# Performance work log

Hardware: AMD Instinct MI355X
Metric: run time of the kernel (lower is better)

## Reference

```python
import jax, jax.numpy as jnp
import numpy as np

D_MODEL = 1024
N_HEADS = 16
HEAD_DIM = D_MODEL // N_HEADS


def setup_inputs() -> dict:
    key = jax.random.key(0)
    ks = jax.random.split(key, 11)
    B, S = 4, 2048
    scale = 1.0 / np.sqrt(D_MODEL)
    inp = {
        "query": jax.random.normal(ks[0], (B, S, D_MODEL), jnp.float32),
        "key": jax.random.normal(ks[1], (B, S, D_MODEL), jnp.float32),
        "value": jax.random.normal(ks[2], (B, S, D_MODEL), jnp.float32),
        "Wq": jax.random.normal(ks[3], (D_MODEL, D_MODEL), jnp.float32) * scale,
        "bq": jnp.zeros((D_MODEL,), jnp.float32),
        "Wk": jax.random.normal(ks[4], (D_MODEL, D_MODEL), jnp.float32) * scale,
        "bk": jnp.zeros((D_MODEL,), jnp.float32),
        "Wv": jax.random.normal(ks[5], (D_MODEL, D_MODEL), jnp.float32) * scale,
        "bv": jnp.zeros((D_MODEL,), jnp.float32),
        "Wo": jax.random.normal(ks[6], (D_MODEL, D_MODEL), jnp.float32) * scale,
        "bo": jnp.zeros((D_MODEL,), jnp.float32),
    }
    return inp


def reference(query, key, value, Wq, bq, Wk, bk, Wv, bv, Wo, bo):
    B, S, _ = query.shape
    # QKV projections (nn.Linear: x @ W.T + b; weights here stored as [out,in])
    q = query @ Wq.T + bq
    k = key @ Wk.T + bk
    v = value @ Wv.T + bv
    # [B, S, H, Dh] -> [B, H, S, Dh]
    q = q.reshape(B, S, N_HEADS, HEAD_DIM).transpose(0, 2, 1, 3)
    k = k.reshape(B, S, N_HEADS, HEAD_DIM).transpose(0, 2, 1, 3)
    v = v.reshape(B, S, N_HEADS, HEAD_DIM).transpose(0, 2, 1, 3)
    # full score matrix [B, H, S, S]
    scores = jnp.einsum("bhqd,bhkd->bhqk", q, k) / jnp.sqrt(
        jnp.asarray(HEAD_DIM, q.dtype)
    )
    attn = jax.nn.softmax(scores, axis=-1)
    out = jnp.einsum("bhqk,bhkd->bhqd", attn, v)  # [B, H, S, Dh]
    out = out.transpose(0, 2, 1, 3).reshape(B, S, D_MODEL)
    return out @ Wo.T + bo
```

## Files before the change

### kernel.cpp

```cpp
#include <hip/hip_runtime.h>
#include <cstdint>
#include <cstddef>


typedef _Float16 h16;
typedef _Float16 h16x4 __attribute__((ext_vector_type(4)));
typedef _Float16 h16x8 __attribute__((ext_vector_type(8)));
typedef __fp16 fp16x2v __attribute__((ext_vector_type(2)));
typedef float f32x4 __attribute__((ext_vector_type(4)));
typedef float f32x16 __attribute__((ext_vector_type(16)));

#define SEQ 2048
#define HDIM 64

__device__ __forceinline__ void gld16(const void* g, void* l) {
  __builtin_amdgcn_global_load_lds((__attribute__((address_space(1))) void*)g,
                                   (__attribute__((address_space(3))) void*)l,
                                   16, 0, 0);
}

#define VMCNT_(n) asm volatile("s_waitcnt vmcnt(" #n ")" ::: "memory")
#define VMCNT(n) VMCNT_(n)

__device__ __forceinline__ void pl32swap(unsigned& a, unsigned& b) {
  asm volatile("v_permlane32_swap_b32 %0, %1" : "+v"(a), "+v"(b));
}

struct CvtArgs {
  const float* src[7];
  h16* dst[7];
  int n4[7];
};

__global__ __launch_bounds__(256) void cvt_kernel(CvtArgs a) {
  const int tk = blockIdx.y;
  const int n4 = a.n4[tk];
  const float4* s = (const float4*)a.src[tk];
  h16x4* d = (h16x4*)a.dst[tk];
  const int stride = gridDim.x * blockDim.x;
  for (int i = blockIdx.x * blockDim.x + threadIdx.x; i < n4; i += stride) {
    float4 v = s[i];
    h16x4 o = {(h16)v.x, (h16)v.y, (h16)v.z, (h16)v.w};
    d[i] = o;
  }
}

enum { EPI_Q = 0, EPI_V = 1, EPI_OUT = 2, EPI_K = 3 };

struct GemmArgs {
  const h16* A[3];
  const h16* W[3];
  const float* bias[3];
  void* dst[3];
  float scale[3];
  int epi[3];
};

__global__ __launch_bounds__(256) void gemm_h16(GemmArgs g) {
  const int z = blockIdx.z;
  const h16* A = g.A[z];
  const h16* W = g.W[z];
  const float* bias = g.bias[z];
  void* dst = g.dst[z];
  const float scale = g.scale[z];
  const int epi = g.epi[z];

  __shared__ __align__(16) h16 sA[128 * 32];
  __shared__ __align__(16) h16 sW[128 * 32];

  const int t = threadIdx.x;
  const int lane = t & 63, wave = t >> 6;
  const int lq = lane & 15, quad = lane >> 4;
  const int wm = wave & 1, wn = wave >> 1;
  const int m0 = blockIdx.y * 128, n0 = blockIdx.x * 128;

  const int srow = wave * 32 + (lane >> 2);
  const int scol = (lane & 3) * 8;
  const h16* Ag = A + (size_t)(m0 + srow) * 1024 + scol;
  const h16* Wg = W + (size_t)(n0 + srow) * 1024 + scol;
  h16* lA = &sA[(wave * 32) * 32];
  h16* lW = &sW[(wave * 32) * 32];

  f32x4 zero4 = {0.f, 0.f, 0.f, 0.f};
  f32x4 acc[4][4];
#pragma unroll
  for (int i = 0; i < 4; ++i)
#pragma unroll
    for (int j = 0; j < 4; ++j) acc[i][j] = zero4;

  for (int k0 = 0; k0 < 1024; k0 += 32) {
    __syncthreads();
    gld16(Ag + k0, lA);
    gld16(Ag + k0 + 16 * 1024, lA + 16 * 32);
    gld16(Wg + k0, lW);
    gld16(Wg + k0 + 16 * 1024, lW + 16 * 32);
    __syncthreads();

    h16x8 af[4], wf[4];
#pragma unroll
    for (int mt = 0; mt < 4; ++mt)
      af[mt] = *(const h16x8*)&sA[(wm * 64 + mt * 16 + lq) * 32 + quad * 8];
#pragma unroll
    for (int nt = 0; nt < 4; ++nt)
      wf[nt] = *(const h16x8*)&sW[(wn * 64 + nt * 16 + lq) * 32 + quad * 8];
#pragma unroll
    for (int mt = 0; mt < 4; ++mt)
#pragma unroll
      for (int nt = 0; nt < 4; ++nt)
        acc[mt][nt] = __builtin_amdgcn_mfma_f32_16x16x32_f16(
            af[mt], wf[nt], acc[mt][nt], 0, 0, 0);
  }

  const int gmb = m0 + wm * 64;
  const int gnb = n0 + wn * 64;
#pragma unroll
  for (int mt = 0; mt < 4; ++mt) {
#pragma unroll
    for (int nt = 0; nt < 4; ++nt) {
      const int gn = gnb + nt * 16 + lq;
      const float bv = bias[gn];
#pragma unroll
      for (int r = 0; r < 4; ++r) {
        const int gm = gmb + mt * 16 + quad * 4 + r;
        const float v = (acc[mt][nt][r] + bv) * scale;
        if (epi == EPI_OUT) {
          ((float*)dst)[(size_t)gm * 1024 + gn] = v;
        } else if (epi == EPI_Q) {
          const int b = gm >> 11, s = gm & 2047, h = gn >> 6, d = gn & 63;
          ((h16*)dst)[((size_t)(b * 16 + h) * 2048 + s) * 64 + d] = (h16)v;
        } else if (epi == EPI_K) {
          const int b = gm >> 11, s = gm & 2047, h = gn >> 6, d = gn & 63;
          const int dsw = (((d >> 3) ^ (s & 7)) << 3) | (d & 7);
          ((h16*)dst)[((size_t)(b * 16 + h) * 2048 + s) * 64 + dsw] = (h16)v;
        } else {
          const int b = gm >> 11, s = gm & 2047, h = gn >> 6, d = gn & 63;
          const int ssw =
              (s & ~127) | (((((s >> 3) & 15) ^ (d & 15))) << 3) | (s & 7);
          ((h16*)dst)[((size_t)(b * 16 + h) * 64 + d) * 2048 + ssw] = (h16)v;
        }
      }
    }
  }
}

__global__ __launch_bounds__(512, 2) void flash_fwd(
    const h16* __restrict__ Qp, const h16* __restrict__ Kp,
    const h16* __restrict__ Vtp, h16* __restrict__ attn) {
  __shared__ __align__(16) h16 sK[2][8192];
  __shared__ __align__(16) h16 sVt[2][8192];

  const int t = threadIdx.x, lane = t & 63, wave = t >> 6;
  const int l31 = lane & 31;
  const int h = lane >> 5;

  const int lin = blockIdx.x + (blockIdx.y << 3);
  const int nid = (lin & 7) * 64 + (lin >> 3);
  const int bh = nid >> 3, q0 = (nid & 7) * 256;

  const h16* Qh = Qp + (size_t)bh * SEQ * HDIM;
  const h16* Kh = Kp + (size_t)bh * SEQ * HDIM;
  const h16* Vh = Vtp + (size_t)bh * HDIM * SEQ;

  const int qrow = q0 + wave * 32 + l31;
  h16x8 bq[4];
#pragma unroll
  for (int ks = 0; ks < 4; ++ks)
    bq[ks] = *(const h16x8*)(Qh + (size_t)qrow * 64 + ks * 16 + h * 8);
  VMCNT(0);
  __builtin_amdgcn_sched_barrier(0);

  const int vr = lane >> 4;
  const int vc = (lane & 15) * 8;

  int colK[4], colV[8];
#pragma unroll
  for (int ks = 0; ks < 4; ++ks) colK[ks] = ((ks * 2 + h) ^ (l31 & 7)) * 8;
#pragma unroll
  for (int ks = 0; ks < 8; ++ks) colV[ks] = ((ks * 2 + h) ^ (l31 & 15)) * 8;

#define STAGE(SLOT, KT)                                                       \
  {                                                                           \
    const h16* gK = Kh + (size_t)(KT) * 64;                                   \
    gld16(gK + wave * 512 + lane * 8, &sK[SLOT][wave * 512]);                 \
    gld16(gK + (wave + 8) * 512 + lane * 8, &sK[SLOT][(wave + 8) * 512]);     \
    gld16(Vh + (size_t)(4 * wave + vr) * SEQ + (KT) + vc,                     \
          &sVt[SLOT][wave * 512]);                                            \
    gld16(Vh + (size_t)(4 * (wave + 8) + vr) * SEQ + (KT) + vc,               \
          &sVt[SLOT][(wave + 8) * 512]);                                      \
  }

  f32x16 zero16 = {};
  f32x16 oT[2];
  oT[0] = zero16;
  oT[1] = zero16;
  float lsum = 0.f;

#define COMPUTE(SLOT)                                                         \
  {                                                                           \
    _Pragma("unroll") for (int mt = 0; mt < 4; ++mt) {                        \
      f32x16 s = zero16;                                                      \
      __builtin_amdgcn_s_setprio(1);                                          \
      _Pragma("unroll") for (int ks = 0; ks < 4; ++ks) {                      \
        h16x8 ak =                                                            \
            *(const h16x8*)&sK[SLOT][(mt * 32 + l31) * 64 + colK[ks]];        \
        s = __builtin_amdgcn_mfma_f32_32x32x16_f16(ak, bq[ks], s, 0, 0, 0);   \
      }                                                                       \
      __builtin_amdgcn_s_setprio(0);                                          \
      uint2 pk[4];                                                            \
      _Pragma("unroll") for (int g = 0; g < 4; ++g) {                         \
        const float e0 = __builtin_amdgcn_exp2f(s[g * 4 + 0]);                \
        const float e1 = __builtin_amdgcn_exp2f(s[g * 4 + 1]);                \
        const float e2 = __builtin_amdgcn_exp2f(s[g * 4 + 2]);                \
        const float e3 = __builtin_amdgcn_exp2f(s[g * 4 + 3]);                \
        lsum += (e0 + e1) + (e2 + e3);                                        \
        fp16x2v c0 = __builtin_amdgcn_cvt_pkrtz(e0, e1);                      \
        fp16x2v c1 = __builtin_amdgcn_cvt_pkrtz(e2, e3);                      \
        pk[g].x = __builtin_bit_cast(unsigned, c0);                           \
        pk[g].y = __builtin_bit_cast(unsigned, c1);                           \
      }                                                                       \
      _Pragma("unroll") for (int ks2 = 0; ks2 < 2; ++ks2) {                   \
        const int ks = mt * 2 + ks2;                                          \
        unsigned ax = pk[2 * ks2].x, ay = pk[2 * ks2].y;                      \
        unsigned bx = pk[2 * ks2 + 1].x, by = pk[2 * ks2 + 1].y;              \
        pl32swap(ax, bx);                                                     \
        pl32swap(ay, by);                                                     \
        uint4 bp32 = {ax, ay, bx, by};                                        \
        h16x8 bp = __builtin_bit_cast(h16x8, bp32);                           \
        __builtin_amdgcn_s_setprio(1);                                        \
        _Pragma("unroll") for (int dt = 0; dt < 2; ++dt) {                    \
          h16x8 av =                                                          \
              *(const h16x8*)&sVt[SLOT][(dt * 32 + l31) * 128 + colV[ks]];    \
          oT[dt] = __builtin_amdgcn_mfma_f32_32x32x16_f16(av, bp, oT[dt], 0,  \
                                                          0, 0);              \
        }                                                                     \
        __builtin_amdgcn_s_setprio(0);                                       \
      }                                                                       \
    }                                                                         \
  }

  STAGE(0, 0);
  STAGE(1, 128);

#pragma unroll 1
  for (int ti = 0; ti < 15; ++ti) {
    VMCNT(4);
    __builtin_amdgcn_s_barrier();
    __builtin_amdgcn_sched_barrier(0);
    const int slot = ti & 1;
    COMPUTE(slot);
    __builtin_amdgcn_sched_barrier(0);
    __builtin_amdgcn_s_barrier();
    if (ti < 14) STAGE(slot, (ti + 2) * 128);
  }
  VMCNT(0);
  __builtin_amdgcn_s_barrier();
  __builtin_amdgcn_sched_barrier(0);
  COMPUTE(1);

#undef STAGE
#undef COMPUTE

  lsum += __shfl_xor(lsum, 32);
  const float inv = 1.f / lsum;

  const int b = bh >> 4, head = bh & 15;
  h16* orow = attn + ((size_t)(b * SEQ + qrow)) * 1024 + head * 64;
#pragma unroll
  for (int dt = 0; dt < 2; ++dt) {
#pragma unroll
    for (int g = 0; g < 4; ++g) {
      h16x4 ov = {(h16)(oT[dt][g * 4 + 0] * inv), (h16)(oT[dt][g * 4 + 1] * inv),
                  (h16)(oT[dt][g * 4 + 2] * inv), (h16)(oT[dt][g * 4 + 3] * inv)};
      *(h16x4*)&orow[dt * 32 + g * 8 + h * 4] = ov;
    }
  }
}

extern "C" void kernel_launch(void* const* d_in, const int* in_sizes, int n_in,
                              void* d_out, int out_size, void* d_ws,
                              size_t ws_size, hipStream_t stream) {
  (void)in_sizes; (void)n_in; (void)out_size;

  const float* query = (const float*)d_in[0];
  const float* key   = (const float*)d_in[1];
  const float* value = (const float*)d_in[2];
  const float* Wq = (const float*)d_in[3];
  const float* bq = (const float*)d_in[4];
  const float* Wk = (const float*)d_in[5];
  const float* bk = (const float*)d_in[6];
  const float* Wv = (const float*)d_in[7];
  const float* bv = (const float*)d_in[8];
  const float* Wo = (const float*)d_in[9];
  const float* bo = (const float*)d_in[10];

  char* ws = (char*)d_ws;
  const size_t MB = 1024 * 1024;
  h16* xq = (h16*)(ws);
  h16* xk = (h16*)(ws + 16 * MB);
  h16* xv = (h16*)(ws + 32 * MB);
  h16* qperm = (h16*)(ws + 48 * MB);
  h16 *kperm, *vperm, *attn, *w16;
  const bool fused = ws_size >= 104 * MB;
  if (fused) {
    kperm = (h16*)(ws + 64 * MB);
    vperm = (h16*)(ws + 80 * MB);
    w16   = (h16*)(ws + 96 * MB);
    attn  = (h16*)(ws);
  } else {
    kperm = (h16*)(ws);
    vperm = (h16*)(ws + 16 * MB);
    attn  = (h16*)(ws + 32 * MB);
    w16   = (h16*)(ws + 64 * MB);
  }
  h16* wq16 = w16;
  h16* wk16 = w16 + 1048576;
  h16* wv16 = w16 + 2 * 1048576;
  h16* wo16 = w16 + 3 * 1048576;

  CvtArgs ca;
  const float* csrc[7] = {query, key, value, Wq, Wk, Wv, Wo};
  h16* cdst[7] = {xq, xk, xv, wq16, wk16, wv16, wo16};
  const int cn4[7] = {2097152, 2097152, 2097152, 262144, 262144, 262144, 262144};
  for (int i = 0; i < 7; ++i) { ca.src[i] = csrc[i]; ca.dst[i] = cdst[i]; ca.n4[i] = cn4[i]; }
  cvt_kernel<<<dim3(512, 7), 256, 0, stream>>>(ca);

  const float qscale = 0.125f * 1.4426950408889634f;
  if (fused) {
    GemmArgs ga;
    ga.A[0] = xq; ga.A[1] = xk; ga.A[2] = xv;
    ga.W[0] = wq16; ga.W[1] = wk16; ga.W[2] = wv16;
    ga.bias[0] = bq; ga.bias[1] = bk; ga.bias[2] = bv;
    ga.dst[0] = qperm; ga.dst[1] = kperm; ga.dst[2] = vperm;
    ga.scale[0] = qscale; ga.scale[1] = 1.f; ga.scale[2] = 1.f;
    ga.epi[0] = EPI_Q; ga.epi[1] = EPI_K; ga.epi[2] = EPI_V;
    gemm_h16<<<dim3(8, 64, 3), 256, 0, stream>>>(ga);
  } else {
    const h16* As[3] = {xq, xk, xv};
    const h16* Ws[3] = {wq16, wk16, wv16};
    const float* bs[3] = {bq, bk, bv};
    h16* ds[3] = {qperm, kperm, vperm};
    const float scl[3] = {qscale, 1.f, 1.f};
    const int ep[3] = {EPI_Q, EPI_K, EPI_V};
    for (int i = 0; i < 3; ++i) {
      GemmArgs ga;
      for (int j = 0; j < 3; ++j) {
        ga.A[j] = As[i]; ga.W[j] = Ws[i]; ga.bias[j] = bs[i];
        ga.dst[j] = ds[i]; ga.scale[j] = scl[i]; ga.epi[j] = ep[i];
      }
      gemm_h16<<<dim3(8, 64, 1), 256, 0, stream>>>(ga);
    }
  }

  flash_fwd<<<dim3(8, 64), 512, 0, stream>>>(qperm, kperm, vperm, attn);

  GemmArgs go;
  for (int j = 0; j < 3; ++j) {
    go.A[j] = attn; go.W[j] = wo16; go.bias[j] = bo;
    go.dst[j] = d_out; go.scale[j] = 1.f; go.epi[j] = EPI_OUT;
  }
  gemm_h16<<<dim3(8, 64, 1), 256, 0, stream>>>(go);
}
```

Baseline: 370.8 us.

## Double-buffer GEMM LDS loads, swizzle LDS layout, and remap blocks across XCDs

The projection GEMM now uses two LDS stages, so global-to-LDS loads for tile k+2 are in flight while tile k is computed. The old single buffer with two syncthreads per iteration is replaced by vmcnt waits and raw s_barriers. The LDS layout gets an XOR swizzle on rows and k-chunks to cut bank conflicts on the fragment reads. Block IDs are remapped so consecutive tiles land on the same XCD for L2 reuse. This doubles LDS usage and relies on precise vmcnt accounting, which is fragile.

```diff
diff --git a/kernel.cpp b/kernel.cpp
--- a/kernel.cpp
+++ b/kernel.cpp
@@ -57,7 +57,19 @@
 };
 
 __global__ __launch_bounds__(256) void gemm_h16(GemmArgs g) {
-  const int z = blockIdx.z;
+  __shared__ __align__(16) h16 sA[2][4096];
+  __shared__ __align__(16) h16 sW[2][4096];
+
+  const int lin =
+      blockIdx.x + gridDim.x * (blockIdx.y + gridDim.y * blockIdx.z);
+  const int total = gridDim.x * gridDim.y * gridDim.z;
+  const int nid = (lin & 7) * (total >> 3) + (lin >> 3);
+  const int per = gridDim.x * gridDim.y;
+  const int z = nid / per;
+  const int r = nid % per;
+  const int n0 = (r % gridDim.x) * 128;
+  const int m0 = (r / gridDim.x) * 128;
+
   const h16* A = g.A[z];
   const h16* W = g.W[z];
   const float* bias = g.bias[z];
@@ -65,21 +77,19 @@
   const float scale = g.scale[z];
   const int epi = g.epi[z];
 
-  __shared__ __align__(16) h16 sA[128 * 32];
-  __shared__ __align__(16) h16 sW[128 * 32];
-
   const int t = threadIdx.x;
   const int lane = t & 63, wave = t >> 6;
   const int lq = lane & 15, quad = lane >> 4;
   const int wm = wave & 1, wn = wave >> 1;
-  const int m0 = blockIdx.y * 128, n0 = blockIdx.x * 128;
-
-  const int srow = wave * 32 + (lane >> 2);
-  const int scol = (lane & 3) * 8;
-  const h16* Ag = A + (size_t)(m0 + srow) * 1024 + scol;
-  const h16* Wg = W + (size_t)(n0 + srow) * 1024 + scol;
-  h16* lA = &sA[(wave * 32) * 32];
-  h16* lW = &sW[(wave * 32) * 32];
+
+  const int bsl = lane >> 2;
+  const int srcRow = (bsl & 14) | ((bsl ^ (bsl >> 2)) & 1);
+  const int srcK = (lane & 3) ^ (srcRow & 3);
+  const h16* AgS = A + (size_t)(m0 + wave * 32 + srcRow) * 1024 + srcK * 8;
+  const h16* WgS = W + (size_t)(n0 + wave * 32 + srcRow) * 1024 + srcK * 8;
+
+  const int rsw = (lq & 14) | ((lq ^ (lq >> 2)) & 1);
+  const int aoff = rsw * 32 + (quad ^ (lq & 3)) * 8;
 
   f32x4 zero4 = {0.f, 0.f, 0.f, 0.f};
   f32x4 acc[4][4];
@@ -88,28 +98,54 @@
 #pragma unroll
     for (int j = 0; j < 4; ++j) acc[i][j] = zero4;
 
-  for (int k0 = 0; k0 < 1024; k0 += 32) {
-    __syncthreads();
-    gld16(Ag + k0, lA);
-    gld16(Ag + k0 + 16 * 1024, lA + 16 * 32);
-    gld16(Wg + k0, lW);
-    gld16(Wg + k0 + 16 * 1024, lW + 16 * 32);
-    __syncthreads();
-
-    h16x8 af[4], wf[4];
-#pragma unroll
-    for (int mt = 0; mt < 4; ++mt)
-      af[mt] = *(const h16x8*)&sA[(wm * 64 + mt * 16 + lq) * 32 + quad * 8];
-#pragma unroll
-    for (int nt = 0; nt < 4; ++nt)
-      wf[nt] = *(const h16x8*)&sW[(wn * 64 + nt * 16 + lq) * 32 + quad * 8];
-#pragma unroll
-    for (int mt = 0; mt < 4; ++mt)
-#pragma unroll
-      for (int nt = 0; nt < 4; ++nt)
-        acc[mt][nt] = __builtin_amdgcn_mfma_f32_16x16x32_f16(
-            af[mt], wf[nt], acc[mt][nt], 0, 0, 0);
-  }
+#define GSTAGE(SLOT, K0)                                                      \
+  {                                                                           \
+    gld16(AgS + (K0), &sA[SLOT][wave * 1024]);                                \
+    gld16(AgS + (K0) + 16 * 1024, &sA[SLOT][wave * 1024 + 512]);              \
+    gld16(WgS + (K0), &sW[SLOT][wave * 1024]);                                \
+    gld16(WgS + (K0) + 16 * 1024, &sW[SLOT][wave * 1024 + 512]);              \
+  }
+
+#define GCOMP(SLOT)                                                           \
+  {                                                                           \
+    h16x8 af[4], wf[4];                                                       \
+    _Pragma("unroll") for (int mt = 0; mt < 4; ++mt) {                        \
+      af[mt] = *(const h16x8*)&sA[SLOT][(wm * 4 + mt) * 512 + aoff];          \
+    }                                                                         \
+    _Pragma("unroll") for (int nt = 0; nt < 4; ++nt) {                        \
+      wf[nt] = *(const h16x8*)&sW[SLOT][(wn * 4 + nt) * 512 + aoff];          \
+    }                                                                         \
+    __builtin_amdgcn_s_setprio(1);                                            \
+    _Pragma("unroll") for (int mt = 0; mt < 4; ++mt) {                        \
+      _Pragma("unroll") for (int nt = 0; nt < 4; ++nt) {                      \
+        acc[mt][nt] = __builtin_amdgcn_mfma_f32_16x16x32_f16(                 \
+            af[mt], wf[nt], acc[mt][nt], 0, 0, 0);                            \
+      }                                                                       \
+    }                                                                         \
+    __builtin_amdgcn_s_setprio(0);                                            \
+  }
+
+  GSTAGE(0, 0);
+  GSTAGE(1, 32);
+
+#pragma unroll 1
+  for (int ti = 0; ti < 31; ++ti) {
+    VMCNT(4);
+    __builtin_amdgcn_s_barrier();
+    __builtin_amdgcn_sched_barrier(0);
+    const int slot = ti & 1;
+    GCOMP(slot);
+    __builtin_amdgcn_sched_barrier(0);
+    __builtin_amdgcn_s_barrier();
+    if (ti < 30) GSTAGE(slot, (ti + 2) * 32);
+  }
+  VMCNT(0);
+  __builtin_amdgcn_s_barrier();
+  __builtin_amdgcn_sched_barrier(0);
+  GCOMP(1);
+
+#undef GSTAGE
+#undef GCOMP
 
   const int gmb = m0 + wm * 64;
   const int gnb = n0 + wn * 64;
@@ -120,9 +156,9 @@
       const int gn = gnb + nt * 16 + lq;
       const float bv = bias[gn];
 #pragma unroll
-      for (int r = 0; r < 4; ++r) {
-        const int gm = gmb + mt * 16 + quad * 4 + r;
-        const float v = (acc[mt][nt][r] + bv) * scale;
+      for (int rr = 0; rr < 4; ++rr) {
+        const int gm = gmb + mt * 16 + quad * 4 + rr;
+        const float v = (acc[mt][nt][rr] + bv) * scale;
         if (epi == EPI_OUT) {
           ((float*)dst)[(size_t)gm * 1024 + gn] = v;
         } else if (epi == EPI_Q) {
```

Measured after the change: 377.2 us. Within noise of the previous version (+1.7%).
